# Performance work log

Hardware: AMD Instinct MI355X
Metric: run time of the kernel (lower is better)

## Reference

```python
import jax, jax.numpy as jnp
import numpy as np

B, LE, LS, DE, DS = 16, 1024, 1024, 1024, 1024


def setup_inputs() -> dict:
    key = jax.random.key(0)
    k1, k2, k3 = jax.random.split(key, 3)
    edit_encodings = jax.random.normal(k1, (B, LE, DE), dtype=jnp.float32)
    src_encodings = jax.random.normal(k2, (B, LS, DS), dtype=jnp.float32)
    # torch nn.Linear(DE, DS, bias=False) weight has shape (DS, DE)
    W = jax.random.normal(k3, (DS, DE), dtype=jnp.float32) * (1.0 / np.sqrt(DE))
    # padding masks: 1 for padding. Per-example valid lengths in [L/2, L].
    edit_lens = np.linspace(LE // 2, LE, B).astype(np.int32)
    src_lens = np.linspace(LS, LS // 2, B).astype(np.int32)
    edit_sent_masks = (np.arange(LE)[None, :] >= edit_lens[:, None]).astype(np.int32)
    src_sent_masks = (np.arange(LS)[None, :] >= src_lens[:, None]).astype(np.int32)
    return {
        "edit_encodings": edit_encodings,
        "src_encodings": src_encodings,
        "edit_sent_masks": jnp.asarray(edit_sent_masks),
        "src_sent_masks": jnp.asarray(src_sent_masks),
        "W": W,
    }


def reference(edit_encodings, src_encodings, edit_sent_masks, src_sent_masks, W):
    # sim: (B, LE, LS) = (edit @ W^T) @ src^T
    proj = jnp.einsum('bed,sd->bes', edit_encodings, W)          # (B, LE, DS)
    sim = jnp.einsum('bes,bls->bel', proj, src_encodings)        # (B, LE, LS)
    neg_inf = jnp.float32(-jnp.inf)
    edit_sim = jnp.where(src_sent_masks[:, None, :].astype(bool), neg_inf, sim)
    src_sim = jnp.where(edit_sent_masks[:, :, None].astype(bool), neg_inf, sim)
    edit_weights = jax.nn.softmax(edit_sim, axis=-1)             # over src positions
    src_weights = jax.nn.softmax(src_sim, axis=1)                # over edit positions
    edit_ctx = jnp.einsum('bel,bls->bes', edit_weights, src_encodings)  # (B, LE, DS)
    src_ctx = jnp.einsum('bel,bed->bld', src_weights, edit_encodings)   # (B, LS, DE)
    return (edit_ctx, src_ctx)
```

## Files before the change

kernel.cpp:

```cpp
#include <hip/hip_runtime.h>
#include <math.h>

#define BATCH 16

typedef __attribute__((ext_vector_type(8))) short s16x8;
typedef __attribute__((ext_vector_type(8))) unsigned short u16x8;
typedef __attribute__((ext_vector_type(4))) float f32x4;

__device__ inline unsigned short f2bf_rn(float f) {
  unsigned u = __float_as_uint(f);
  u += 0x7FFF + ((u >> 16) & 1);
  return (unsigned short)(u >> 16);
}
__device__ inline float bf2f(unsigned short h) {
  return __uint_as_float(((unsigned)h) << 16);
}

__device__ __forceinline__ void gload16(const unsigned short* g, unsigned short* l) {
  __builtin_amdgcn_global_load_lds(
      (__attribute__((address_space(1))) void*)g,
      (__attribute__((address_space(3))) void*)l, 16, 0, 0);
}

__global__ __launch_bounds__(256) void cvt_split(
    const float* __restrict__ X, unsigned short* __restrict__ H,
    unsigned short* __restrict__ L) {
  const size_t i = (((size_t)blockIdx.x << 8) + threadIdx.x) << 2;
  f32x4 v = *(const f32x4*)(X + i);
  ushort4 h, l;
  h.x = f2bf_rn(v[0]); l.x = f2bf_rn(v[0] - bf2f(h.x));
  h.y = f2bf_rn(v[1]); l.y = f2bf_rn(v[1] - bf2f(h.y));
  h.z = f2bf_rn(v[2]); l.z = f2bf_rn(v[2] - bf2f(h.z));
  h.w = f2bf_rn(v[3]); l.w = f2bf_rn(v[3] - bf2f(h.w));
  *(ushort4*)(H + i) = h;
  *(ushort4*)(L + i) = l;
}

__global__ __launch_bounds__(256) void cvt_split2(
    const float* __restrict__ X0, unsigned short* __restrict__ H0,
    unsigned short* __restrict__ L0, const float* __restrict__ X1,
    unsigned short* __restrict__ H1, unsigned short* __restrict__ L1) {
  const int bid = blockIdx.x;
  const float* X;
  unsigned short *H, *L;
  size_t base;
  if (bid < 16384) { X = X0; H = H0; L = L0; base = (size_t)bid << 8; }
  else { X = X1; H = H1; L = L1; base = (size_t)(bid - 16384) << 8; }
  const size_t i = (base + threadIdx.x) << 2;
  f32x4 v = *(const f32x4*)(X + i);
  ushort4 h, l;
  h.x = f2bf_rn(v[0]); l.x = f2bf_rn(v[0] - bf2f(h.x));
  h.y = f2bf_rn(v[1]); l.y = f2bf_rn(v[1] - bf2f(h.y));
  h.z = f2bf_rn(v[2]); l.z = f2bf_rn(v[2] - bf2f(h.z));
  h.w = f2bf_rn(v[3]); l.w = f2bf_rn(v[3] - bf2f(h.w));
  *(ushort4*)(H + i) = h;
  *(ushort4*)(L + i) = l;
}

template <int HILO, int SPLIT_OUT>
__global__ __launch_bounds__(512, 2) void gemm8p(
    const unsigned short* __restrict__ AH, const unsigned short* __restrict__ AL,
    const unsigned short* __restrict__ BH, const unsigned short* __restrict__ BL,
    void* __restrict__ Cout, void* __restrict__ CoutL,
    long long sA, long long sB, long long sC, int batched) {
  constexpr int NARR = HILO ? 4 : 2;
  __shared__ __align__(16) unsigned short lds[2][NARR][8192];
  const int tid = threadIdx.x;
  const int wg = ((blockIdx.x & 7) << 5) | (blockIdx.x >> 3);
  int z, bm, bn;
  if (batched) {
    z = wg >> 4; bm = ((wg >> 2) & 3) << 8; bn = (wg & 3) << 8;
  } else {
    z = 0; bm = (wg >> 2) << 8; bn = (wg & 3) << 8;
  }
  const int wave = tid >> 6, lane = tid & 63;
  const int wm = wave >> 2, wn = wave & 3;
  const int fr = lane & 15, fks = lane >> 4;

  const int svrow = tid >> 2;
  const int scol = ((tid & 3) ^ ((tid >> 3) & 3)) << 3;
  const unsigned short* gA0 = AH + (size_t)z * sA + (size_t)(bm + svrow) * 1024 + scol;
  const unsigned short* gB0 = BH + (size_t)z * sB + (size_t)(bn + svrow) * 1024 + scol;
  const unsigned short* gA1 = HILO ? (AL + (size_t)z * sA + (size_t)(bm + svrow) * 1024 + scol) : gA0;
  const unsigned short* gB1 = HILO ? (BL + (size_t)z * sB + (size_t)(bn + svrow) * 1024 + scol) : gB0;
  const int lwb = wave << 9;

  int aoff[8], boff[4];
#pragma unroll
  for (int m = 0; m < 8; m++) {
    const int r = (wm << 7) + (m << 4) + fr;
    aoff[m] = (r << 5) + ((fks ^ ((r >> 1) & 3)) << 3);
  }
#pragma unroll
  for (int n = 0; n < 4; n++) {
    const int r = (wn << 6) + (n << 4) + fr;
    boff[n] = (r << 5) + ((fks ^ ((r >> 1) & 3)) << 3);
  }

  f32x4 acc[8][4];
#pragma unroll
  for (int m = 0; m < 8; m++)
#pragma unroll
    for (int n = 0; n < 4; n++) acc[m][n] = (f32x4)(0.f);

#define ISS(NXT, ARR, G, Q, KO) \
  gload16((G) + ((size_t)(Q) << 17) + (KO), &lds[NXT][ARR][((Q) << 12) + lwb])

  ISS(0, 0, gA0, 0, 0); ISS(0, 0, gA0, 1, 0);
  ISS(0, 1, gB0, 0, 0); ISS(0, 1, gB0, 1, 0);
  if (HILO) {
    ISS(0, 2, gA1, 0, 0); ISS(0, 2, gA1, 1, 0);
    ISS(0, 3, gB1, 0, 0); ISS(0, 3, gB1, 1, 0);
  }
  __syncthreads();

#pragma unroll 1
  for (int kt = 0; kt < 32; ++kt) {
    const int cur = kt & 1, nxt = cur ^ 1;
    const int kn = (kt + 1) << 5;
    const bool pf = kt < 31;
    const unsigned short* LAH = lds[cur][0];
    const unsigned short* LBH = lds[cur][1];
    const unsigned short* LAL = lds[cur][HILO ? 2 : 0];
    const unsigned short* LBL = lds[cur][HILO ? 3 : 1];
    s16x8 ah[4], al[4], bh[2], bl[2];

#define LDA8(QM)                                                         \
  do {                                                                   \
    _Pragma("unroll") for (int m_ = 0; m_ < 4; m_++) {                   \
      const int o_ = aoff[((QM) << 2) + m_];                             \
      ah[m_] = *(const s16x8*)&LAH[o_];                                  \
      if (HILO) al[m_] = *(const s16x8*)&LAL[o_];                        \
    }                                                                    \
  } while (0)
#define LDB4(QN)                                                         \
  do {                                                                   \
    _Pragma("unroll") for (int n_ = 0; n_ < 2; n_++) {                   \
      const int o_ = boff[((QN) << 1) + n_];                             \
      bh[n_] = *(const s16x8*)&LBH[o_];                                  \
      if (HILO) bl[n_] = *(const s16x8*)&LBL[o_];                        \
    }                                                                    \
  } while (0)
#define MM8(QM, QN)                                                              \
  do {                                                                           \
    _Pragma("unroll") for (int m_ = 0; m_ < 4; m_++)                             \
        _Pragma("unroll") for (int n_ = 0; n_ < 2; n_++) {                       \
      const int M_ = ((QM) << 2) + m_, N_ = ((QN) << 1) + n_;                    \
      if (HILO) {                                                                \
        acc[M_][N_] = __builtin_amdgcn_mfma_f32_16x16x32_bf16(al[m_], bh[n_],    \
                                                              acc[M_][N_], 0, 0, 0); \
        acc[M_][N_] = __builtin_amdgcn_mfma_f32_16x16x32_bf16(ah[m_], bl[n_],    \
                                                              acc[M_][N_], 0, 0, 0); \
      }                                                                          \
      acc[M_][N_] = __builtin_amdgcn_mfma_f32_16x16x32_bf16(ah[m_], bh[n_],      \
                                                            acc[M_][N_], 0, 0, 0);   \
    }                                                                            \
  } while (0)

    LDA8(0); LDB4(0);
    if (pf) {
      ISS(nxt, 0, gA0, 0, kn); ISS(nxt, 0, gA0, 1, kn);
      if (HILO) { ISS(nxt, 2, gA1, 0, kn); ISS(nxt, 2, gA1, 1, kn); }
    }
    __builtin_amdgcn_s_barrier();
    __builtin_amdgcn_s_setprio(1); MM8(0, 0); __builtin_amdgcn_s_setprio(0);
    __builtin_amdgcn_s_barrier();

    LDB4(1);
    if (pf) {
      ISS(nxt, 1, gB0, 0, kn); ISS(nxt, 1, gB0, 1, kn);
      if (HILO) { ISS(nxt, 3, gB1, 0, kn); ISS(nxt, 3, gB1, 1, kn); }
    }
    __builtin_amdgcn_s_barrier();
    __builtin_amdgcn_s_setprio(1); MM8(0, 1); __builtin_amdgcn_s_setprio(0);
    __builtin_amdgcn_s_barrier();

    LDA8(1); LDB4(0);
    __builtin_amdgcn_s_barrier();
    __builtin_amdgcn_s_setprio(1); MM8(1, 0); __builtin_amdgcn_s_setprio(0);
    __builtin_amdgcn_s_barrier();

    LDB4(1);
    __builtin_amdgcn_s_barrier();
    __builtin_amdgcn_s_setprio(1); MM8(1, 1); __builtin_amdgcn_s_setprio(0);
    __syncthreads();
#undef LDA8
#undef LDB4
#undef MM8
  }
#undef ISS

  const int cr = (lane >> 4) << 2;
  const int crow0 = bm + (wm << 7);
  const int ccol0 = bn + (wn << 6);
  if (SPLIT_OUT) {
    unsigned short* CH = (unsigned short*)Cout + (size_t)z * sC;
    unsigned short* CL = (unsigned short*)CoutL + (size_t)z * sC;
#pragma unroll
    for (int m = 0; m < 8; m++)
#pragma unroll
      for (int r = 0; r < 4; r++) {
        const size_t base = (size_t)(crow0 + (m << 4) + cr + r) * 1024 + ccol0 + fr;
#pragma unroll
        for (int n = 0; n < 4; n++) {
          float f = acc[m][n][r];
          unsigned short h = f2bf_rn(f);
          CH[base + (n << 4)] = h;
          CL[base + (n << 4)] = f2bf_rn(f - bf2f(h));
        }
      }
  } else {
    float* C = (float*)Cout + (size_t)z * sC;
#pragma unroll
    for (int m = 0; m < 8; m++)
#pragma unroll
      for (int r = 0; r < 4; r++) {
        float* cp = C + (size_t)(crow0 + (m << 4) + cr + r) * 1024 + ccol0 + fr;
#pragma unroll
        for (int n = 0; n < 4; n++) cp[n << 4] = acc[m][n][r];
      }
  }
}

__device__ inline float waveMax(float v) {
#pragma unroll
  for (int o = 32; o > 0; o >>= 1) v = fmaxf(v, __shfl_down(v, o, 64));
  return v;
}
__device__ inline float waveSum(float v) {
#pragma unroll
  for (int o = 32; o > 0; o >>= 1) v += __shfl_down(v, o, 64);
  return v;
}

__global__ __launch_bounds__(256) void row_softmax_kernel(
    const float* __restrict__ sim, const int* __restrict__ smask,
    unsigned short* __restrict__ out) {
  const int row = blockIdx.x;
  const int b = row >> 10;
  const float* x = sim + ((size_t)row << 10);
  const int* mk = smask + (b << 10);
  const int t = threadIdx.x;

  float4 v = ((const float4*)x)[t];
  int4 m = ((const int4*)mk)[t];
  float vv[4] = {v.x, v.y, v.z, v.w};
  const int mmv[4] = {m.x, m.y, m.z, m.w};

  float mx = -3.0e38f;
#pragma unroll
  for (int i = 0; i < 4; i++)
    if (!mmv[i]) mx = fmaxf(mx, vv[i]);

  __shared__ float red[4];
  float wmx = waveMax(mx);
  const int wave = t >> 6;
  if ((t & 63) == 0) red[wave] = wmx;
  __syncthreads();
  mx = fmaxf(fmaxf(red[0], red[1]), fmaxf(red[2], red[3]));
  __syncthreads();

  float s = 0.f;
#pragma unroll
  for (int i = 0; i < 4; i++) {
    float e = mmv[i] ? 0.f : __expf(vv[i] - mx);
    vv[i] = e;
    s += e;
  }
  float ws = waveSum(s);
  if ((t & 63) == 0) red[wave] = ws;
  __syncthreads();
  s = red[0] + red[1] + red[2] + red[3];
  float inv = 1.0f / s;

  ushort4 o;
  o.x = f2bf_rn(vv[0] * inv);
  o.y = f2bf_rn(vv[1] * inv);
  o.z = f2bf_rn(vv[2] * inv);
  o.w = f2bf_rn(vv[3] * inv);
  *(ushort4*)&out[((size_t)row << 10) + (t << 2)] = o;
}

__global__ __launch_bounds__(256) void col_partial(
    const float* __restrict__ sim, const int* __restrict__ emask,
    float* __restrict__ pmax, float* __restrict__ psum) {
  const int b = blockIdx.z;
  const int ec = blockIdx.y;
  const int l = (blockIdx.x << 8) + threadIdx.x;
  const float* p = sim + ((size_t)b << 20) + (((size_t)ec << 6) << 10) + l;
  const int* mk = emask + (b << 10) + (ec << 6);
  float mx0 = -1.0e30f, s0 = 0.f, mx1 = -1.0e30f, s1 = 0.f;
#pragma unroll 4
  for (int i = 0; i < 64; i += 2) {
    float v0 = mk[i] ? -3.0e38f : p[(size_t)i << 10];
    float v1 = mk[i + 1] ? -3.0e38f : p[(size_t)(i + 1) << 10];
    float n0 = fmaxf(mx0, v0);
    s0 = s0 * __expf(mx0 - n0) + __expf(v0 - n0);
    mx0 = n0;
    float n1 = fmaxf(mx1, v1);
    s1 = s1 * __expf(mx1 - n1) + __expf(v1 - n1);
    mx1 = n1;
  }
  float M = fmaxf(mx0, mx1);
  float S = s0 * __expf(mx0 - M) + s1 * __expf(mx1 - M);
  const int o = (((b << 4) + ec) << 10) + l;
  pmax[o] = M;
  psum[o] = S;
}

__global__ __launch_bounds__(256) void col_weights_T(
    const float* __restrict__ sim, const int* __restrict__ emask,
    const float* __restrict__ pmax, const float* __restrict__ psum,
    unsigned short* __restrict__ wT) {
  const int b = blockIdx.z;
  const int l0 = blockIdx.x << 6;
  const int e0 = blockIdx.y << 6;
  const int t = threadIdx.x;
  __shared__ float Ml[64], Il[64];
  __shared__ int msk[64];
  __shared__ float gm[4][64], gs[4][64];
  __shared__ unsigned short tile[64][72];

  {
    const int ll = t & 63, g = t >> 6;
    float m = -1.0e30f, s = 0.f;
#pragma unroll
    for (int q = 0; q < 4; q++) {
      int ec = g + (q << 2);
      const int o = (((b << 4) + ec) << 10) + l0 + ll;
      float pm = pmax[o], ps = psum[o];
      float nm = fmaxf(m, pm);
      s = s * __expf(m - nm) + ps * __expf(pm - nm);
      m = nm;
    }
    gm[g][ll] = m;
    gs[g][ll] = s;
    __syncthreads();
    if (t < 64) {
      float M = fmaxf(fmaxf(gm[0][t], gm[1][t]), fmaxf(gm[2][t], gm[3][t]));
      float S = 0.f;
#pragma unroll
      for (int q = 0; q < 4; q++) S += gs[q][t] * __expf(gm[q][t] - M);
      Ml[t] = M;
      Il[t] = 1.0f / S;
      msk[t] = emask[(b << 10) + e0 + t];
    }
    __syncthreads();
  }

  const int lane = t & 63, wv = t >> 6;
#pragma unroll
  for (int i = 0; i < 16; i++) {
    const int el = (wv << 4) + i;
    float v = sim[((size_t)b << 20) + ((size_t)(e0 + el) << 10) + l0 + lane];
    float w = msk[el] ? 0.f : __expf(v - Ml[lane]) * Il[lane];
    tile[lane][el] = f2bf_rn(w);
  }
  __syncthreads();
  const int r = t >> 2, seg = (t & 3) << 4;
  u16x8 v0 = *(const u16x8*)&tile[r][seg];
  u16x8 v1 = *(const u16x8*)&tile[r][seg + 8];
  size_t o = ((size_t)((b << 10) + l0 + r) << 10) + e0 + seg;
  *(u16x8*)&wT[o] = v0;
  *(u16x8*)&wT[o + 8] = v1;
}

__global__ __launch_bounds__(256) void transpose16d(
    const unsigned short* __restrict__ X0, unsigned short* __restrict__ T0,
    const unsigned short* __restrict__ X1, unsigned short* __restrict__ T1) {
  __shared__ unsigned short ts[64][72];
  const int zz = blockIdx.z;
  const int b = zz & 15;
  const unsigned short* Xb = (zz < 16 ? X0 : X1) + ((size_t)b << 20);
  unsigned short* Tb = (zz < 16 ? T0 : T1) + ((size_t)b << 20);
  const int d0 = blockIdx.x << 6, l0 = blockIdx.y << 6;
  const int t = threadIdx.x;
  const int row = t >> 2, seg = (t & 3) << 4;
  u16x8 v0 = *(const u16x8*)&Xb[((size_t)(l0 + row) << 10) + d0 + seg];
  u16x8 v1 = *(const u16x8*)&Xb[((size_t)(l0 + row) << 10) + d0 + seg + 8];
#pragma unroll
  for (int i = 0; i < 8; i++) ts[seg + i][row] = v0[i];
#pragma unroll
  for (int i = 0; i < 8; i++) ts[seg + 8 + i][row] = v1[i];
  __syncthreads();
  u16x8 o0 = *(const u16x8*)&ts[row][seg];
  u16x8 o1 = *(const u16x8*)&ts[row][seg + 8];
  size_t o = ((size_t)(d0 + row) << 10) + l0 + seg;
  *(u16x8*)&Tb[o] = o0;
  *(u16x8*)&Tb[o + 8] = o1;
}

extern "C" void kernel_launch(void* const* d_in, const int* in_sizes, int n_in,
                              void* d_out, int out_size, void* d_ws,
                              size_t ws_size, hipStream_t stream) {
  const float* edit = (const float*)d_in[0];
  const float* src = (const float*)d_in[1];
  const int* emask = (const int*)d_in[2];
  const int* smask = (const int*)d_in[3];
  const float* W = (const float*)d_in[4];

  char* ws = (char*)d_ws;
  char* dob = (char*)d_out;

  unsigned short* eH = (unsigned short*)ws;
  unsigned short* sH = (unsigned short*)(ws + ((size_t)32 << 20));
  unsigned short* pH = (unsigned short*)(ws + ((size_t)64 << 20));
  unsigned short* pL = (unsigned short*)(ws + ((size_t)96 << 20));
  unsigned short* wE = pH;
  unsigned short* wST = pL;
  unsigned short* editT = sH;

  unsigned short* eL = (unsigned short*)dob;
  unsigned short* sL = (unsigned short*)(dob + ((size_t)64 << 20));
  unsigned short* WH = (unsigned short*)(dob + ((size_t)96 << 20));
  unsigned short* WL = (unsigned short*)(dob + ((size_t)98 << 20));
  float* sim = (float*)dob;
  float* pmax = (float*)(dob + ((size_t)64 << 20));
  float* psum = (float*)(dob + ((size_t)65 << 20));
  unsigned short* srcT = (unsigned short*)(dob + ((size_t)64 << 20));
  float* out_edit = (float*)dob;
  float* out_src = (float*)(dob + ((size_t)64 << 20));

  const long long S1 = 1LL << 20;
  dim3 blk(256), blk512(512);

  cvt_split2<<<dim3(32768), blk, 0, stream>>>(edit, eH, eL, src, sH, sL);
  cvt_split<<<dim3(1024), blk, 0, stream>>>(W, WH, WL);

  gemm8p<1, 1><<<dim3(256), blk512, 0, stream>>>(
      eH, eL, WH, WL, (void*)pH, (void*)pL, 0, 0, 0, 0);

  gemm8p<1, 0><<<dim3(256), blk512, 0, stream>>>(
      pH, pL, sH, sL, (void*)sim, nullptr, S1, S1, S1, 1);

  row_softmax_kernel<<<dim3(BATCH << 10), blk, 0, stream>>>(sim, smask, wE);
  col_partial<<<dim3(4, 16, BATCH), blk, 0, stream>>>(sim, emask, pmax, psum);
  col_weights_T<<<dim3(16, 16, BATCH), blk, 0, stream>>>(sim, emask, pmax, psum, wST);

  transpose16d<<<dim3(16, 16, 32), blk, 0, stream>>>(sH, srcT, eH, editT);

  gemm8p<0, 0><<<dim3(256), blk512, 0, stream>>>(
      wE, nullptr, srcT, nullptr, (void*)out_edit, nullptr, S1, S1, S1, 1);
  gemm8p<0, 0><<<dim3(256), blk512, 0, stream>>>(
      wST, nullptr, editT, nullptr, (void*)out_src, nullptr, S1, S1, S1, 1);
}
```

Measured before the change: 549.7 us.

## Restructure GEMM inner loop into two phases, merge conversion kernels, split transpose

The GEMM main loop moves from four sub-phases to two. All B fragments are loaded once per k-step, all next-tile prefetches are issued up front, and each phase runs a 4x4 block of MFMAs with the hi/lo correction terms grouped first. This cuts barriers and LDS re-reads of B per k-step but holds more fragment registers, which could raise register pressure at launch bounds 512,2. The W conversion is folded into the single split-conversion launch to save one kernel launch. The combined transpose is split back into two launches, which reads as a cleanup rather than a speed change.

New measurement: 551.1 us. About the same (+0.3%).

```diff
diff --git a/kernel.cpp b/kernel.cpp
--- a/kernel.cpp
+++ b/kernel.cpp
@@ -22,30 +22,19 @@
       (__attribute__((address_space(3))) void*)l, 16, 0, 0);
 }
 
-__global__ __launch_bounds__(256) void cvt_split(
-    const float* __restrict__ X, unsigned short* __restrict__ H,
-    unsigned short* __restrict__ L) {
-  const size_t i = (((size_t)blockIdx.x << 8) + threadIdx.x) << 2;
-  f32x4 v = *(const f32x4*)(X + i);
-  ushort4 h, l;
-  h.x = f2bf_rn(v[0]); l.x = f2bf_rn(v[0] - bf2f(h.x));
-  h.y = f2bf_rn(v[1]); l.y = f2bf_rn(v[1] - bf2f(h.y));
-  h.z = f2bf_rn(v[2]); l.z = f2bf_rn(v[2] - bf2f(h.z));
-  h.w = f2bf_rn(v[3]); l.w = f2bf_rn(v[3] - bf2f(h.w));
-  *(ushort4*)(H + i) = h;
-  *(ushort4*)(L + i) = l;
-}
-
-__global__ __launch_bounds__(256) void cvt_split2(
+__global__ __launch_bounds__(256) void cvt_split3(
     const float* __restrict__ X0, unsigned short* __restrict__ H0,
     unsigned short* __restrict__ L0, const float* __restrict__ X1,
-    unsigned short* __restrict__ H1, unsigned short* __restrict__ L1) {
+    unsigned short* __restrict__ H1, unsigned short* __restrict__ L1,
+    const float* __restrict__ X2, unsigned short* __restrict__ H2,
+    unsigned short* __restrict__ L2) {
   const int bid = blockIdx.x;
   const float* X;
   unsigned short *H, *L;
   size_t base;
   if (bid < 16384) { X = X0; H = H0; L = L0; base = (size_t)bid << 8; }
-  else { X = X1; H = H1; L = L1; base = (size_t)(bid - 16384) << 8; }
+  else if (bid < 32768) { X = X1; H = H1; L = L1; base = (size_t)(bid - 16384) << 8; }
+  else { X = X2; H = H2; L = L2; base = (size_t)(bid - 32768) << 8; }
   const size_t i = (base + threadIdx.x) << 2;
   f32x4 v = *(const f32x4*)(X + i);
   ushort4 h, l;
@@ -123,9 +112,9 @@
     const unsigned short* LBH = lds[cur][1];
     const unsigned short* LAL = lds[cur][HILO ? 2 : 0];
     const unsigned short* LBL = lds[cur][HILO ? 3 : 1];
-    s16x8 ah[4], al[4], bh[2], bl[2];
-
-#define LDA8(QM)                                                         \
+    s16x8 ah[4], al[4], bh[4], bl[4];
+
+#define LDA4(QM)                                                         \
   do {                                                                   \
     _Pragma("unroll") for (int m_ = 0; m_ < 4; m_++) {                   \
       const int o_ = aoff[((QM) << 2) + m_];                             \
@@ -133,60 +122,55 @@
       if (HILO) al[m_] = *(const s16x8*)&LAL[o_];                        \
     }                                                                    \
   } while (0)
-#define LDB4(QN)                                                         \
+#define LDBALL()                                                         \
   do {                                                                   \
-    _Pragma("unroll") for (int n_ = 0; n_ < 2; n_++) {                   \
-      const int o_ = boff[((QN) << 1) + n_];                             \
+    _Pragma("unroll") for (int n_ = 0; n_ < 4; n_++) {                   \
+      const int o_ = boff[n_];                                           \
       bh[n_] = *(const s16x8*)&LBH[o_];                                  \
       if (HILO) bl[n_] = *(const s16x8*)&LBL[o_];                        \
     }                                                                    \
   } while (0)
-#define MM8(QM, QN)                                                              \
+#define MMQ(QM)                                                                  \
   do {                                                                           \
+    if (HILO) {                                                                  \
+      _Pragma("unroll") for (int m_ = 0; m_ < 4; m_++)                           \
+          _Pragma("unroll") for (int n_ = 0; n_ < 4; n_++)                       \
+              acc[((QM) << 2) + m_][n_] =                                        \
+          __builtin_amdgcn_mfma_f32_16x16x32_bf16(al[m_], bh[n_],                \
+                                                  acc[((QM) << 2) + m_][n_], 0, 0, 0); \
+      _Pragma("unroll") for (int m_ = 0; m_ < 4; m_++)                           \
+          _Pragma("unroll") for (int n_ = 0; n_ < 4; n_++)                       \
+              acc[((QM) << 2) + m_][n_] =                                        \
+          __builtin_amdgcn_mfma_f32_16x16x32_bf16(ah[m_], bl[n_],                \
+                                                  acc[((QM) << 2) + m_][n_], 0, 0, 0); \
+    }                                                                            \
     _Pragma("unroll") for (int m_ = 0; m_ < 4; m_++)                             \
-        _Pragma("unroll") for (int n_ = 0; n_ < 2; n_++) {                       \
-      const int M_ = ((QM) << 2) + m_, N_ = ((QN) << 1) + n_;                    \
-      if (HILO) {                                                                \
-        acc[M_][N_] = __builtin_amdgcn_mfma_f32_16x16x32_bf16(al[m_], bh[n_],    \
-                                                              acc[M_][N_], 0, 0, 0); \
-        acc[M_][N_] = __builtin_amdgcn_mfma_f32_16x16x32_bf16(ah[m_], bl[n_],    \
-                                                              acc[M_][N_], 0, 0, 0); \
-      }                                                                          \
-      acc[M_][N_] = __builtin_amdgcn_mfma_f32_16x16x32_bf16(ah[m_], bh[n_],      \
-                                                            acc[M_][N_], 0, 0, 0);   \
-    }                                                                            \
+        _Pragma("unroll") for (int n_ = 0; n_ < 4; n_++)                         \
+            acc[((QM) << 2) + m_][n_] =                                          \
+        __builtin_amdgcn_mfma_f32_16x16x32_bf16(ah[m_], bh[n_],                  \
+                                                acc[((QM) << 2) + m_][n_], 0, 0, 0);   \
   } while (0)
 
-    LDA8(0); LDB4(0);
+    LDA4(0); LDBALL();
     if (pf) {
       ISS(nxt, 0, gA0, 0, kn); ISS(nxt, 0, gA0, 1, kn);
-      if (HILO) { ISS(nxt, 2, gA1, 0, kn); ISS(nxt, 2, gA1, 1, kn); }
+      ISS(nxt, 1, gB0, 0, kn); ISS(nxt, 1, gB0, 1, kn);
+      if (HILO) {
+        ISS(nxt, 2, gA1, 0, kn); ISS(nxt, 2, gA1, 1, kn);
+        ISS(nxt, 3, gB1, 0, kn); ISS(nxt, 3, gB1, 1, kn);
+      }
     }
     __builtin_amdgcn_s_barrier();
-    __builtin_amdgcn_s_setprio(1); MM8(0, 0); __builtin_amdgcn_s_setprio(0);
+    __builtin_amdgcn_s_setprio(1); MMQ(0); __builtin_amdgcn_s_setprio(0);
     __builtin_amdgcn_s_barrier();
 
-    LDB4(1);
-    if (pf) {
-      ISS(nxt, 1, gB0, 0, kn); ISS(nxt, 1, gB0, 1, kn);
-      if (HILO) { ISS(nxt, 3, gB1, 0, kn); ISS(nxt, 3, gB1, 1, kn); }
-    }
+    LDA4(1);
     __builtin_amdgcn_s_barrier();
-    __builtin_amdgcn_s_setprio(1); MM8(0, 1); __builtin_amdgcn_s_setprio(0);
-    __builtin_amdgcn_s_barrier();
-
-    LDA8(1); LDB4(0);
-    __builtin_amdgcn_s_barrier();
-    __builtin_amdgcn_s_setprio(1); MM8(1, 0); __builtin_amdgcn_s_setprio(0);
-    __builtin_amdgcn_s_barrier();
-
-    LDB4(1);
-    __builtin_amdgcn_s_barrier();
-    __builtin_amdgcn_s_setprio(1); MM8(1, 1); __builtin_amdgcn_s_setprio(0);
+    __builtin_amdgcn_s_setprio(1); MMQ(1); __builtin_amdgcn_s_setprio(0);
     __syncthreads();
-#undef LDA8
-#undef LDB4
-#undef MM8
+#undef LDA4
+#undef LDBALL
+#undef MMQ
   }
 #undef ISS
 
@@ -365,16 +349,14 @@
   *(u16x8*)&wT[o + 8] = v1;
 }
 
-__global__ __launch_bounds__(256) void transpose16d(
-    const unsigned short* __restrict__ X0, unsigned short* __restrict__ T0,
-    const unsigned short* __restrict__ X1, unsigned short* __restrict__ T1) {
+__global__ __launch_bounds__(256) void transpose16(
+    const unsigned short* __restrict__ X, unsigned short* __restrict__ XT) {
   __shared__ unsigned short ts[64][72];
-  const int zz = blockIdx.z;
-  const int b = zz & 15;
-  const unsigned short* Xb = (zz < 16 ? X0 : X1) + ((size_t)b << 20);
-  unsigned short* Tb = (zz < 16 ? T0 : T1) + ((size_t)b << 20);
+  const int b = blockIdx.z;
   const int d0 = blockIdx.x << 6, l0 = blockIdx.y << 6;
   const int t = threadIdx.x;
+  const unsigned short* Xb = X + ((size_t)b << 20);
+  unsigned short* Tb = XT + ((size_t)b << 20);
   const int row = t >> 2, seg = (t & 3) << 4;
   u16x8 v0 = *(const u16x8*)&Xb[((size_t)(l0 + row) << 10) + d0 + seg];
   u16x8 v1 = *(const u16x8*)&Xb[((size_t)(l0 + row) << 10) + d0 + seg + 8];
@@ -424,8 +406,7 @@
   const long long S1 = 1LL << 20;
   dim3 blk(256), blk512(512);
 
-  cvt_split2<<<dim3(32768), blk, 0, stream>>>(edit, eH, eL, src, sH, sL);
-  cvt_split<<<dim3(1024), blk, 0, stream>>>(W, WH, WL);
+  cvt_split3<<<dim3(33792), blk, 0, stream>>>(edit, eH, eL, src, sH, sL, W, WH, WL);
 
   gemm8p<1, 1><<<dim3(256), blk512, 0, stream>>>(
       eH, eL, WH, WL, (void*)pH, (void*)pL, 0, 0, 0, 0);
@@ -437,7 +418,8 @@
   col_partial<<<dim3(4, 16, BATCH), blk, 0, stream>>>(sim, emask, pmax, psum);
   col_weights_T<<<dim3(16, 16, BATCH), blk, 0, stream>>>(sim, emask, pmax, psum, wST);
 
-  transpose16d<<<dim3(16, 16, 32), blk, 0, stream>>>(sH, srcT, eH, editT);
+  transpose16<<<dim3(16, 16, BATCH), blk, 0, stream>>>(sH, srcT);
+  transpose16<<<dim3(16, 16, BATCH), blk, 0, stream>>>(eH, editT);
 
   gemm8p<0, 0><<<dim3(256), blk512, 0, stream>>>(
       wE, nullptr, srcT, nullptr, (void*)out_edit, nullptr, S1, S1, S1, 1);
```
